# Optimization experiments

Hardware: AMD Instinct MI355X
Metric: run time of the kernel (lower is better)

The kernel has to match this reference:

```python
import jax, jax.numpy as jnp
import numpy as np

B, S, D, H = 2, 2048, 1024, 16
DK = D // H


def setup_inputs() -> dict:
    key = jax.random.key(0)
    ks = jax.random.split(key, 11)
    scale = jnp.float32(1.0 / np.sqrt(D))
    inp = {
        "query": jax.random.normal(ks[0], (B, S, D), jnp.float32),
        "key": jax.random.normal(ks[1], (B, S, D), jnp.float32),
        "value": jax.random.normal(ks[2], (B, S, D), jnp.float32),
        # causal mask: True = masked (masked_fill semantics), broadcast over batch/heads
        "mask": jnp.triu(jnp.ones((S, S), dtype=bool), k=1)[None, None, :, :],
        "Wq": jax.random.normal(ks[3], (D, D), jnp.float32) * scale,
        "bq": jnp.zeros((D,), jnp.float32),
        "Wk": jax.random.normal(ks[4], (D, D), jnp.float32) * scale,
        "bk": jnp.zeros((D,), jnp.float32),
        "Wv": jax.random.normal(ks[5], (D, D), jnp.float32) * scale,
        "bv": jnp.zeros((D,), jnp.float32),
        "Wo": jax.random.normal(ks[6], (D, D), jnp.float32) * scale,
        "bo": jnp.zeros((D,), jnp.float32),
    }
    return inp


def _split_heads(x):
    # (B, S, D) -> (B, H, S, DK)
    b, s, _ = x.shape
    return x.reshape(b, s, H, DK).transpose(0, 2, 1, 3)


def reference(query, key, value, mask, Wq, bq, Wk, bk, Wv, bv, Wo, bo):
    # nn.Linear: y = x @ W.T + b
    q = _split_heads(query @ Wq.T + bq)
    k = _split_heads(key @ Wk.T + bk)
    v = _split_heads(value @ Wv.T + bv)

    inv_sqrt_dk = jnp.float32(1.0 / np.sqrt(DK))
    scores = jnp.einsum("bhqd,bhkd->bhqk", q, k) * inv_sqrt_dk  # (B,H,S,S)
    scores = jnp.where(mask, jnp.float32(-jnp.inf), scores)
    weights = jax.nn.softmax(scores, axis=-1)
    weights = jnp.nan_to_num(weights, nan=0.0)  # fully-masked rows -> 0

    attn = jnp.einsum("bhqk,bhkd->bhqd", weights, v)  # (B,H,S,DK)
    merged = attn.transpose(0, 2, 1, 3).reshape(B, S, D)  # merge heads
    return merged @ Wo.T + bo
```

## Files before the change

kernel.cpp:

```cpp
#include <hip/hip_runtime.h>


typedef unsigned short u16;
typedef unsigned int u32;
typedef __attribute__((ext_vector_type(8))) __bf16 bf16x8;
typedef __attribute__((ext_vector_type(8))) unsigned short us8;
typedef __attribute__((ext_vector_type(4))) float f32x4;

#define S_LEN 2048
#define D_DIM 1024
#define NH 16
#define DKH 64
#define Mi 1048576ULL

__device__ __forceinline__ u16 f2bf(float f) {
  return __builtin_bit_cast(u16, (__bf16)f);
}
__device__ __forceinline__ bf16x8 ld_frag(const u16* p) {
  us8 v = *(const us8*)p;
  return __builtin_bit_cast(bf16x8, v);
}
__device__ __forceinline__ float fast_exp2(float x) {
  float r;
  asm("v_exp_f32 %0, %1" : "=v"(r) : "v"(x));
  return r;
}
__device__ __forceinline__ void gl2lds16(const u16* g, u16* l) {
  __builtin_amdgcn_global_load_lds(
      (__attribute__((address_space(1))) void*)(g),
      (__attribute__((address_space(3))) void*)(l), 16, 0, 0);
}

__global__ __launch_bounds__(256, 1) void cvt_all(
    const float* __restrict__ q, const float* __restrict__ k, const float* __restrict__ v,
    const float* __restrict__ wq, const float* __restrict__ wk,
    const float* __restrict__ wv, const float* __restrict__ wo,
    u16* __restrict__ dst, u32* __restrict__ cnt)
{
  if (blockIdx.x == 0 && threadIdx.x == 0) *cnt = 0;
  size_t e0 = ((size_t)blockIdx.x * 256 + threadIdx.x) * 8;
  const float* s;
  if      (e0 <  4*Mi) s = q  + e0;
  else if (e0 <  8*Mi) s = k  + (e0 - 4*Mi);
  else if (e0 < 12*Mi) s = v  + (e0 - 8*Mi);
  else if (e0 < 13*Mi) s = wq + (e0 - 12*Mi);
  else if (e0 < 14*Mi) s = wk + (e0 - 13*Mi);
  else if (e0 < 15*Mi) s = wv + (e0 - 14*Mi);
  else                 s = wo + (e0 - 15*Mi);
  float4 a = ((const float4*)s)[0];
  float4 b = ((const float4*)s)[1];
  us8 o;
  o[0]=f2bf(a.x); o[1]=f2bf(a.y); o[2]=f2bf(a.z); o[3]=f2bf(a.w);
  o[4]=f2bf(b.x); o[5]=f2bf(b.y); o[6]=f2bf(b.z); o[7]=f2bf(b.w);
  *(us8*)(dst + e0) = o;
}

__global__ __launch_bounds__(256, 1) void gemm_qkv_bb(
    const u16* __restrict__ Aq, const u16* __restrict__ Ak, const u16* __restrict__ Av,
    const u16* __restrict__ Wqb, const u16* __restrict__ Wkb, const u16* __restrict__ Wvb,
    const float* __restrict__ bq, const float* __restrict__ bk, const float* __restrict__ bv,
    u16* __restrict__ Oq, u16* __restrict__ Ok, u16* __restrict__ Ov, float qscale)
{
  const int z = blockIdx.z;
  const u16* A = (z == 0) ? Aq : (z == 1) ? Ak : Av;
  const u16* W = (z == 0) ? Wqb : (z == 1) ? Wkb : Wvb;
  const float* bias = (z == 0) ? bq : (z == 1) ? bk : bv;
  u16* out = (z == 0) ? Oq : (z == 1) ? Ok : Ov;
  const float scale = (z == 0) ? qscale : 1.0f;
  const int K = 1024;

  __shared__ u16 lA[128 * 32];
  __shared__ u16 lB[128 * 32];
  const int t = threadIdx.x;
  const int w = t >> 6, l = t & 63;
  const int mblk = blockIdx.y * 128, nblk = blockIdx.x * 128;
  const int wm = (w & 1) * 64, wn = (w >> 1) * 64;
  const int lr = l & 15, lq = l >> 4;
  const int srow = l >> 2, scol = (l & 3) * 8;

  f32x4 acc[4][4] = {};

  for (int k0 = 0; k0 < K; k0 += 32) {
    __syncthreads();
    #pragma unroll
    for (int r = 0; r < 2; ++r) {
      int grp = r * 4 + w;
      gl2lds16(A + (size_t)(mblk + grp * 16 + srow) * K + k0 + scol, &lA[grp * 512]);
      gl2lds16(W + (size_t)(nblk + grp * 16 + srow) * K + k0 + scol, &lB[grp * 512]);
    }
    __syncthreads();
    bf16x8 aF[4], bF[4];
    #pragma unroll
    for (int mt = 0; mt < 4; ++mt)
      aF[mt] = ld_frag(&lA[(wm + mt * 16 + lr) * 32 + lq * 8]);
    #pragma unroll
    for (int nt = 0; nt < 4; ++nt)
      bF[nt] = ld_frag(&lB[(wn + nt * 16 + lr) * 32 + lq * 8]);
    #pragma unroll
    for (int mt = 0; mt < 4; ++mt)
      #pragma unroll
      for (int nt = 0; nt < 4; ++nt)
        acc[mt][nt] = __builtin_amdgcn_mfma_f32_16x16x32_bf16(aF[mt], bF[nt], acc[mt][nt], 0, 0, 0);
  }

  #pragma unroll
  for (int mt = 0; mt < 4; ++mt)
    #pragma unroll
    for (int nt = 0; nt < 4; ++nt)
      #pragma unroll
      for (int r = 0; r < 4; ++r) {
        int rowg = mblk + wm + mt * 16 + lq * 4 + r;
        int colg = nblk + wn + nt * 16 + lr;
        float v = (acc[mt][nt][r] + bias[colg]) * scale;
        int b = rowg >> 11, s = rowg & 2047;
        int h = colg >> 6, dk = colg & 63;
        if (z != 2)
          out[(((size_t)(b * NH + h)) * S_LEN + s) * DKH + dk] = f2bf(v);
        else
          out[(((size_t)(b * NH + h)) * DKH + dk) * S_LEN + s] = f2bf(v);
      }
}

__global__ __launch_bounds__(256, 1) void gemm_out_bb(
    const u16* __restrict__ A, const u16* __restrict__ W,
    const float* __restrict__ bias, float* __restrict__ out)
{
  const int K = 1024;
  __shared__ u16 lA[128 * 64];
  __shared__ u16 lB[64 * 64];
  const int bid = blockIdx.x;
  const int o   = (bid & 7) * 64 + (bid >> 3);
  const int mblk = (o >> 4) * 128, nblk = (o & 15) * 64;
  const int t = threadIdx.x;
  const int w = t >> 6, l = t & 63;
  const int wm = (w & 1) * 64, wn = (w >> 1) * 32;
  const int lr = l & 15, lq = l >> 4;
  const int srow = l >> 3;
  const int sgr  = (l & 7) ^ srow;

  f32x4 acc[4][2] = {};

  for (int k0 = 0; k0 < K; k0 += 64) {
    __syncthreads();
    #pragma unroll
    for (int i = 0; i < 4; ++i) {
      int chunk = w * 4 + i;
      int row = chunk * 8 + srow;
      gl2lds16(A + (size_t)(mblk + row) * K + k0 + sgr * 8, &lA[chunk * 512]);
    }
    #pragma unroll
    for (int i = 0; i < 2; ++i) {
      int chunk = w * 2 + i;
      int row = chunk * 8 + srow;
      gl2lds16(W + (size_t)(nblk + row) * K + k0 + sgr * 8, &lB[chunk * 512]);
    }
    __syncthreads();
    #pragma unroll
    for (int kk = 0; kk < 2; ++kk) {
      bf16x8 aF[4], bF[2];
      #pragma unroll
      for (int mt = 0; mt < 4; ++mt)
        aF[mt] = ld_frag(&lA[(wm + mt * 16 + lr) * 64 + ((kk * 4 + lq) ^ (lr & 7)) * 8]);
      #pragma unroll
      for (int nt = 0; nt < 2; ++nt)
        bF[nt] = ld_frag(&lB[(wn + nt * 16 + lr) * 64 + ((kk * 4 + lq) ^ (lr & 7)) * 8]);
      #pragma unroll
      for (int mt = 0; mt < 4; ++mt)
        #pragma unroll
        for (int nt = 0; nt < 2; ++nt)
          acc[mt][nt] = __builtin_amdgcn_mfma_f32_16x16x32_bf16(aF[mt], bF[nt], acc[mt][nt], 0, 0, 0);
    }
  }

  #pragma unroll
  for (int mt = 0; mt < 4; ++mt)
    #pragma unroll
    for (int nt = 0; nt < 2; ++nt)
      #pragma unroll
      for (int r = 0; r < 4; ++r) {
        int rowg = mblk + wm + mt * 16 + lq * 4 + r;
        int colg = nblk + wn + nt * 16 + lr;
        out[(size_t)rowg * D_DIM + colg] = acc[mt][nt][r] + bias[colg];
      }
}

__global__ __launch_bounds__(256, 1) void attn_fused(
    const u16* __restrict__ Q, const u16* __restrict__ K,
    const u16* __restrict__ Vt, u16* __restrict__ O, u32* __restrict__ cnt)
{
  __shared__ u16 lK[3][64 * 64];
  __shared__ u16 lV[3][64 * 64];
  __shared__ int s_item;

  const int t = threadIdx.x;
  const int w = t >> 6, l = t & 63;
  const int lr = l & 15, lq = l >> 4;
  const int srow8 = l >> 3;
  const int schunk = l & 7;

  #define STAGE(T, bsel)                                                          \
    do {                                                                          \
      _Pragma("unroll")                                                           \
      for (int r2 = 0; r2 < 2; ++r2) {                                            \
        int grp = r2 * 4 + w;                                                     \
        int row = grp * 8 + srow8;                                                \
        int sw = (row & 3) | (((row >> 3) & 1) << 2);                             \
        int c = schunk ^ sw;                                                      \
        gl2lds16(Kp + (size_t)((T) * 64 + row) * DKH + c * 8, &lK[bsel][grp * 512]); \
        gl2lds16(Vp + (size_t)row * S_LEN + (T) * 64 + c * 8, &lV[bsel][grp * 512]); \
      }                                                                           \
    } while (0)

  while (true) {
    __syncthreads();
    if (t == 0) s_item = (int)atomicAdd(cnt, 1u);
    __syncthreads();
    const int item = s_item;
    if (item >= 1024) break;
    const int qt = 31 - (item >> 5);
    const int bh = item & 31;
    const int b = bh >> 4, h = bh & 15;

    const u16* Qp = Q + (size_t)bh * S_LEN * DKH;
    const u16* Kp = K + (size_t)bh * S_LEN * DKH;
    const u16* Vp = Vt + (size_t)bh * DKH * S_LEN;

    const int qrow = qt * 64 + w * 16 + lr;
    bf16x8 qf[2];
    qf[0] = ld_frag(Qp + (size_t)qrow * DKH + lq * 8);
    qf[1] = ld_frag(Qp + (size_t)qrow * DKH + 32 + lq * 8);

    f32x4 o4[4] = {};
    f32x4 li4 = {};

    STAGE(0, 0);
    if (qt >= 1) STAGE(1, 1);

    for (int kt = 0; kt < qt; ++kt) {
      const int cur = kt % 3;
      asm volatile("s_waitcnt vmcnt(4)\n\ts_barrier" ::: "memory");
      if (kt + 2 <= qt) STAGE(kt + 2, (kt + 2) % 3);

      f32x4 st[4] = {};
      #pragma unroll
      for (int ksd = 0; ksd < 2; ++ksd)
        #pragma unroll
        for (int nt = 0; nt < 4; ++nt) {
          int sig = 32 * (nt >> 1) + 8 * (lr >> 2) + 4 * (nt & 1) + (lr & 3);
          int slot = (ksd * 4 + lq) ^ (lr & 7);
          bf16x8 kb = ld_frag(&lK[cur][sig * 64 + slot * 8]);
          st[nt] = __builtin_amdgcn_mfma_f32_16x16x32_bf16(kb, qf[ksd], st[nt], 0, 0, 0);
        }

      float p[4][4];
      #pragma unroll
      for (int nt = 0; nt < 4; ++nt)
        #pragma unroll
        for (int r = 0; r < 4; ++r) {
          p[nt][r] = fast_exp2(st[nt][r]);
          li4[r] += p[nt][r];
        }

      #pragma unroll
      for (int ks = 0; ks < 2; ++ks) {
        us8 av;
        #pragma unroll
        for (int j = 0; j < 4; ++j) {
          av[j] = f2bf(p[2 * ks][j]);
          av[4 + j] = f2bf(p[2 * ks + 1][j]);
        }
        bf16x8 pa = __builtin_bit_cast(bf16x8, av);
        #pragma unroll
        for (int dblk = 0; dblk < 4; ++dblk) {
          int d = dblk * 16 + lr;
          int sw = (d & 3) | (((d >> 3) & 1) << 2);
          int slot = (4 * ks + lq) ^ sw;
          bf16x8 vb = ld_frag(&lV[cur][d * 64 + slot * 8]);
          o4[dblk] = __builtin_amdgcn_mfma_f32_16x16x32_bf16(pa, vb, o4[dblk], 0, 0, 0);
        }
      }
    }

    {
      const int cur = qt % 3;
      asm volatile("s_waitcnt vmcnt(0)\n\ts_barrier" ::: "memory");
      f32x4 st[4] = {};
      #pragma unroll
      for (int ksd = 0; ksd < 2; ++ksd)
        #pragma unroll
        for (int nt = 0; nt < 4; ++nt) {
          int sig = 32 * (nt >> 1) + 8 * (lr >> 2) + 4 * (nt & 1) + (lr & 3);
          int slot = (ksd * 4 + lq) ^ (lr & 7);
          bf16x8 kb = ld_frag(&lK[cur][sig * 64 + slot * 8]);
          st[nt] = __builtin_amdgcn_mfma_f32_16x16x32_bf16(kb, qf[ksd], st[nt], 0, 0, 0);
        }

      float p[4][4];
      const int qloc = w * 16 + lr;
      #pragma unroll
      for (int nt = 0; nt < 4; ++nt)
        #pragma unroll
        for (int r = 0; r < 4; ++r) {
          int kk = 32 * (nt >> 1) + 8 * lq + 4 * (nt & 1) + r;
          float e = fast_exp2(st[nt][r]);
          p[nt][r] = (kk > qloc) ? 0.0f : e;
          li4[r] += p[nt][r];
        }

      #pragma unroll
      for (int ks = 0; ks < 2; ++ks) {
        us8 av;
        #pragma unroll
        for (int j = 0; j < 4; ++j) {
          av[j] = f2bf(p[2 * ks][j]);
          av[4 + j] = f2bf(p[2 * ks + 1][j]);
        }
        bf16x8 pa = __builtin_bit_cast(bf16x8, av);
        #pragma unroll
        for (int dblk = 0; dblk < 4; ++dblk) {
          int d = dblk * 16 + lr;
          int sw = (d & 3) | (((d >> 3) & 1) << 2);
          int slot = (4 * ks + lq) ^ sw;
          bf16x8 vb = ld_frag(&lV[cur][d * 64 + slot * 8]);
          o4[dblk] = __builtin_amdgcn_mfma_f32_16x16x32_bf16(pa, vb, o4[dblk], 0, 0, 0);
        }
      }
    }

    float li = li4[0] + li4[1] + li4[2] + li4[3];
    li += __shfl_xor(li, 16);
    li += __shfl_xor(li, 32);
    float ri[4];
    #pragma unroll
    for (int r = 0; r < 4; ++r) ri[r] = 1.0f / __shfl(li, lq * 4 + r);

    const size_t obase = ((size_t)b * S_LEN + qt * 64 + w * 16) * D_DIM + h * DKH;
    #pragma unroll
    for (int dblk = 0; dblk < 4; ++dblk)
      #pragma unroll
      for (int r = 0; r < 4; ++r)
        O[obase + (size_t)(lq * 4 + r) * D_DIM + dblk * 16 + lr] = f2bf(o4[dblk][r] * ri[r]);
  }
  #undef STAGE
}

extern "C" void kernel_launch(void* const* d_in, const int* in_sizes, int n_in,
                              void* d_out, int out_size, void* d_ws, size_t ws_size,
                              hipStream_t stream) {
  const float* query = (const float*)d_in[0];
  const float* key   = (const float*)d_in[1];
  const float* value = (const float*)d_in[2];
  const float* Wq = (const float*)d_in[4];
  const float* bq = (const float*)d_in[5];
  const float* Wk = (const float*)d_in[6];
  const float* bk = (const float*)d_in[7];
  const float* Wv = (const float*)d_in[8];
  const float* bv = (const float*)d_in[9];
  const float* Wo = (const float*)d_in[10];
  const float* bo = (const float*)d_in[11];
  float* out = (float*)d_out;

  const float qscale = 0.125f * 1.44269504088896341f;
  dim3 blk(256);

  u16* base = (u16*)d_ws;
  u16* Qb = base;
  u16* Kb = base + 4 * Mi;
  u16* Vb = base + 8 * Mi;

  u16* cvt = base + 12 * Mi;
  u16* qbf = cvt;
  u16* kbf = cvt + 4 * Mi;
  u16* vbf = cvt + 8 * Mi;
  u16* wqb = cvt + 12 * Mi;
  u16* wkb = cvt + 13 * Mi;
  u16* wvb = cvt + 14 * Mi;
  u16* wob = cvt + 15 * Mi;
  u16* Ab  = qbf;

  u32* cnt = (u32*)d_out;

  cvt_all<<<dim3(8192), blk, 0, stream>>>(query, key, value, Wq, Wk, Wv, Wo, cvt, cnt);
  gemm_qkv_bb<<<dim3(8, 32, 3), blk, 0, stream>>>(qbf, kbf, vbf, wqb, wkb, wvb,
                                                  bq, bk, bv, Qb, Kb, Vb, qscale);
  attn_fused<<<dim3(768), blk, 0, stream>>>(Qb, Kb, Vb, Ab, cnt);
  gemm_out_bb<<<dim3(512), blk, 0, stream>>>(Ab, wob, bo, out);
}
```

Measured before the change: 230.6 us.

## Process paired query tiles per attention work item and remap QKV GEMM blocks

Each attention work item now handles two adjacent 64-row query tiles, so every staged K/V tile in LDS is reused by both query tiles. This halves the K/V global loads and barrier/sync overhead per query row. In exchange it doubles accumulator registers and coarsens the dynamic work items (512 instead of 1024), which can hurt load balance. The QKV GEMM grid is also flattened to 1D with a remapping that spreads consecutive block IDs across z and tiles, probably to spread the work across XCDs or improve cache locality.

```diff
diff --git a/kernel.cpp b/kernel.cpp
--- a/kernel.cpp
+++ b/kernel.cpp
@@ -61,7 +61,13 @@
     const float* __restrict__ bq, const float* __restrict__ bk, const float* __restrict__ bv,
     u16* __restrict__ Oq, u16* __restrict__ Ok, u16* __restrict__ Ov, float qscale)
 {
-  const int z = blockIdx.z;
+  const int bid = blockIdx.x;
+  const int o   = (bid & 7) * 96 + (bid >> 3);
+  const int z   = o >> 8;
+  const int rem = o & 255;
+  const int mblk = (rem >> 3) * 128;
+  const int nblk = (rem & 7) * 128;
+
   const u16* A = (z == 0) ? Aq : (z == 1) ? Ak : Av;
   const u16* W = (z == 0) ? Wqb : (z == 1) ? Wkb : Wvb;
   const float* bias = (z == 0) ? bq : (z == 1) ? bk : bv;
@@ -73,7 +79,6 @@
   __shared__ u16 lB[128 * 32];
   const int t = threadIdx.x;
   const int w = t >> 6, l = t & 63;
-  const int mblk = blockIdx.y * 128, nblk = blockIdx.x * 128;
   const int wm = (w & 1) * 64, wn = (w >> 1) * 64;
   const int lr = l & 15, lq = l >> 4;
   const int srow = l >> 2, scol = (l & 3) * 8;
@@ -211,37 +216,124 @@
       }                                                                           \
     } while (0)
 
+  #define QKT_PAIR(cur, stA, stB)                                                 \
+    do {                                                                          \
+      _Pragma("unroll")                                                           \
+      for (int ksd = 0; ksd < 2; ++ksd)                                           \
+        _Pragma("unroll")                                                         \
+        for (int nt = 0; nt < 4; ++nt) {                                          \
+          int sig = 32 * (nt >> 1) + 8 * (lr >> 2) + 4 * (nt & 1) + (lr & 3);     \
+          int slot = (ksd * 4 + lq) ^ (lr & 7);                                   \
+          bf16x8 kb = ld_frag(&lK[cur][sig * 64 + slot * 8]);                     \
+          stA[nt] = __builtin_amdgcn_mfma_f32_16x16x32_bf16(kb, qfA[ksd], stA[nt], 0, 0, 0); \
+          stB[nt] = __builtin_amdgcn_mfma_f32_16x16x32_bf16(kb, qfB[ksd], stB[nt], 0, 0, 0); \
+        }                                                                         \
+    } while (0)
+
+  #define PV_PAIR(cur, avA, avB)                                                  \
+    do {                                                                          \
+      _Pragma("unroll")                                                           \
+      for (int ks = 0; ks < 2; ++ks) {                                            \
+        bf16x8 paA = __builtin_bit_cast(bf16x8, avA[ks]);                         \
+        bf16x8 paB = __builtin_bit_cast(bf16x8, avB[ks]);                         \
+        _Pragma("unroll")                                                         \
+        for (int dblk = 0; dblk < 4; ++dblk) {                                    \
+          int d = dblk * 16 + lr;                                                 \
+          int sw = (d & 3) | (((d >> 3) & 1) << 2);                               \
+          int slot = (4 * ks + lq) ^ sw;                                          \
+          bf16x8 vb = ld_frag(&lV[cur][d * 64 + slot * 8]);                       \
+          o4A[dblk] = __builtin_amdgcn_mfma_f32_16x16x32_bf16(paA, vb, o4A[dblk], 0, 0, 0); \
+          o4B[dblk] = __builtin_amdgcn_mfma_f32_16x16x32_bf16(paB, vb, o4B[dblk], 0, 0, 0); \
+        }                                                                         \
+      }                                                                           \
+    } while (0)
+
   while (true) {
     __syncthreads();
     if (t == 0) s_item = (int)atomicAdd(cnt, 1u);
     __syncthreads();
     const int item = s_item;
-    if (item >= 1024) break;
-    const int qt = 31 - (item >> 5);
+    if (item >= 512) break;
+    const int j  = 15 - (item >> 5);
     const int bh = item & 31;
+    const int qta = 2 * j, qtb = 2 * j + 1;
     const int b = bh >> 4, h = bh & 15;
 
     const u16* Qp = Q + (size_t)bh * S_LEN * DKH;
     const u16* Kp = K + (size_t)bh * S_LEN * DKH;
     const u16* Vp = Vt + (size_t)bh * DKH * S_LEN;
 
-    const int qrow = qt * 64 + w * 16 + lr;
-    bf16x8 qf[2];
-    qf[0] = ld_frag(Qp + (size_t)qrow * DKH + lq * 8);
-    qf[1] = ld_frag(Qp + (size_t)qrow * DKH + 32 + lq * 8);
-
-    f32x4 o4[4] = {};
-    f32x4 li4 = {};
+    const int qrowA = qta * 64 + w * 16 + lr;
+    const int qrowB = qtb * 64 + w * 16 + lr;
+    bf16x8 qfA[2], qfB[2];
+    qfA[0] = ld_frag(Qp + (size_t)qrowA * DKH + lq * 8);
+    qfA[1] = ld_frag(Qp + (size_t)qrowA * DKH + 32 + lq * 8);
+    qfB[0] = ld_frag(Qp + (size_t)qrowB * DKH + lq * 8);
+    qfB[1] = ld_frag(Qp + (size_t)qrowB * DKH + 32 + lq * 8);
+
+    f32x4 o4A[4] = {}, o4B[4] = {};
+    f32x4 liA = {}, liB = {};
 
     STAGE(0, 0);
-    if (qt >= 1) STAGE(1, 1);
-
-    for (int kt = 0; kt < qt; ++kt) {
+    STAGE(1, 1);
+
+    for (int kt = 0; kt < qta; ++kt) {
       const int cur = kt % 3;
       asm volatile("s_waitcnt vmcnt(4)\n\ts_barrier" ::: "memory");
-      if (kt + 2 <= qt) STAGE(kt + 2, (kt + 2) % 3);
-
-      f32x4 st[4] = {};
+      if (kt + 2 <= qtb) STAGE(kt + 2, (kt + 2) % 3);
+
+      f32x4 stA[4] = {}, stB[4] = {};
+      QKT_PAIR(cur, stA, stB);
+
+      us8 avA[2], avB[2];
+      #pragma unroll
+      for (int ks = 0; ks < 2; ++ks)
+        #pragma unroll
+        for (int rr = 0; rr < 4; ++rr) {
+          float eA0 = fast_exp2(stA[2 * ks][rr]);
+          float eA1 = fast_exp2(stA[2 * ks + 1][rr]);
+          float eB0 = fast_exp2(stB[2 * ks][rr]);
+          float eB1 = fast_exp2(stB[2 * ks + 1][rr]);
+          liA[rr] += eA0 + eA1;
+          liB[rr] += eB0 + eB1;
+          avA[ks][rr] = f2bf(eA0); avA[ks][4 + rr] = f2bf(eA1);
+          avB[ks][rr] = f2bf(eB0); avB[ks][4 + rr] = f2bf(eB1);
+        }
+      PV_PAIR(cur, avA, avB);
+    }
+
+    {
+      const int cur = qta % 3;
+      asm volatile("s_waitcnt vmcnt(4)\n\ts_barrier" ::: "memory");
+
+      f32x4 stA[4] = {}, stB[4] = {};
+      QKT_PAIR(cur, stA, stB);
+
+      const int qloc = w * 16 + lr;
+      us8 avA[2], avB[2];
+      #pragma unroll
+      for (int ks = 0; ks < 2; ++ks)
+        #pragma unroll
+        for (int rr = 0; rr < 4; ++rr) {
+          int kk0 = 32 * ks + 8 * lq + rr;
+          int kk1 = 32 * ks + 8 * lq + 4 + rr;
+          float eA0 = (kk0 > qloc) ? 0.0f : fast_exp2(stA[2 * ks][rr]);
+          float eA1 = (kk1 > qloc) ? 0.0f : fast_exp2(stA[2 * ks + 1][rr]);
+          float eB0 = fast_exp2(stB[2 * ks][rr]);
+          float eB1 = fast_exp2(stB[2 * ks + 1][rr]);
+          liA[rr] += eA0 + eA1;
+          liB[rr] += eB0 + eB1;
+          avA[ks][rr] = f2bf(eA0); avA[ks][4 + rr] = f2bf(eA1);
+          avB[ks][rr] = f2bf(eB0); avB[ks][4 + rr] = f2bf(eB1);
+        }
+      PV_PAIR(cur, avA, avB);
+    }
+
+    {
+      const int cur = qtb % 3;
+      asm volatile("s_waitcnt vmcnt(0)\n\ts_barrier" ::: "memory");
+
+      f32x4 stB[4] = {};
       #pragma unroll
       for (int ksd = 0; ksd < 2; ++ksd)
         #pragma unroll
@@ -249,99 +341,62 @@
           int sig = 32 * (nt >> 1) + 8 * (lr >> 2) + 4 * (nt & 1) + (lr & 3);
           int slot = (ksd * 4 + lq) ^ (lr & 7);
           bf16x8 kb = ld_frag(&lK[cur][sig * 64 + slot * 8]);
-          st[nt] = __builtin_amdgcn_mfma_f32_16x16x32_bf16(kb, qf[ksd], st[nt], 0, 0, 0);
+          stB[nt] = __builtin_amdgcn_mfma_f32_16x16x32_bf16(kb, qfB[ksd], stB[nt], 0, 0, 0);
         }
 
-      float p[4][4];
-      #pragma unroll
-      for (int nt = 0; nt < 4; ++nt)
-        #pragma unroll
-        for (int r = 0; r < 4; ++r) {
-          p[nt][r] = fast_exp2(st[nt][r]);
-          li4[r] += p[nt][r];
+      const int qloc = w * 16 + lr;
+      us8 avB[2];
+      #pragma unroll
+      for (int ks = 0; ks < 2; ++ks)
+        #pragma unroll
+        for (int rr = 0; rr < 4; ++rr) {
+          int kk0 = 32 * ks + 8 * lq + rr;
+          int kk1 = 32 * ks + 8 * lq + 4 + rr;
+          float eB0 = (kk0 > qloc) ? 0.0f : fast_exp2(stB[2 * ks][rr]);
+          float eB1 = (kk1 > qloc) ? 0.0f : fast_exp2(stB[2 * ks + 1][rr]);
+          liB[rr] += eB0 + eB1;
+          avB[ks][rr] = f2bf(eB0); avB[ks][4 + rr] = f2bf(eB1);
         }
-
       #pragma unroll
       for (int ks = 0; ks < 2; ++ks) {
-        us8 av;
-        #pragma unroll
-        for (int j = 0; j < 4; ++j) {
-          av[j] = f2bf(p[2 * ks][j]);
-          av[4 + j] = f2bf(p[2 * ks + 1][j]);
-        }
-        bf16x8 pa = __builtin_bit_cast(bf16x8, av);
+        bf16x8 paB = __builtin_bit_cast(bf16x8, avB[ks]);
         #pragma unroll
         for (int dblk = 0; dblk < 4; ++dblk) {
           int d = dblk * 16 + lr;
           int sw = (d & 3) | (((d >> 3) & 1) << 2);
           int slot = (4 * ks + lq) ^ sw;
           bf16x8 vb = ld_frag(&lV[cur][d * 64 + slot * 8]);
-          o4[dblk] = __builtin_amdgcn_mfma_f32_16x16x32_bf16(pa, vb, o4[dblk], 0, 0, 0);
+          o4B[dblk] = __builtin_amdgcn_mfma_f32_16x16x32_bf16(paB, vb, o4B[dblk], 0, 0, 0);
         }
       }
     }
 
-    {
-      const int cur = qt % 3;
-      asm volatile("s_waitcnt vmcnt(0)\n\ts_barrier" ::: "memory");
-      f32x4 st[4] = {};
-      #pragma unroll
-      for (int ksd = 0; ksd < 2; ++ksd)
-        #pragma unroll
-        for (int nt = 0; nt < 4; ++nt) {
-          int sig = 32 * (nt >> 1) + 8 * (lr >> 2) + 4 * (nt & 1) + (lr & 3);
-          int slot = (ksd * 4 + lq) ^ (lr & 7);
-          bf16x8 kb = ld_frag(&lK[cur][sig * 64 + slot * 8]);
-          st[nt] = __builtin_amdgcn_mfma_f32_16x16x32_bf16(kb, qf[ksd], st[nt], 0, 0, 0);
-        }
-
-      float p[4][4];
-      const int qloc = w * 16 + lr;
-      #pragma unroll
-      for (int nt = 0; nt < 4; ++nt)
-        #pragma unroll
-        for (int r = 0; r < 4; ++r) {
-          int kk = 32 * (nt >> 1) + 8 * lq + 4 * (nt & 1) + r;
-          float e = fast_exp2(st[nt][r]);
-          p[nt][r] = (kk > qloc) ? 0.0f : e;
-          li4[r] += p[nt][r];
-        }
-
-      #pragma unroll
-      for (int ks = 0; ks < 2; ++ks) {
-        us8 av;
-        #pragma unroll
-        for (int j = 0; j < 4; ++j) {
-          av[j] = f2bf(p[2 * ks][j]);
-          av[4 + j] = f2bf(p[2 * ks + 1][j]);
-        }
-        bf16x8 pa = __builtin_bit_cast(bf16x8, av);
-        #pragma unroll
-        for (int dblk = 0; dblk < 4; ++dblk) {
-          int d = dblk * 16 + lr;
-          int sw = (d & 3) | (((d >> 3) & 1) << 2);
-          int slot = (4 * ks + lq) ^ sw;
-          bf16x8 vb = ld_frag(&lV[cur][d * 64 + slot * 8]);
-          o4[dblk] = __builtin_amdgcn_mfma_f32_16x16x32_bf16(pa, vb, o4[dblk], 0, 0, 0);
-        }
+    float lA_ = liA[0] + liA[1] + liA[2] + liA[3];
+    lA_ += __shfl_xor(lA_, 16);
+    lA_ += __shfl_xor(lA_, 32);
+    float lB_ = liB[0] + liB[1] + liB[2] + liB[3];
+    lB_ += __shfl_xor(lB_, 16);
+    lB_ += __shfl_xor(lB_, 32);
+    float riA[4], riB[4];
+    #pragma unroll
+    for (int r = 0; r < 4; ++r) {
+      riA[r] = 1.0f / __shfl(lA_, lq * 4 + r);
+      riB[r] = 1.0f / __shfl(lB_, lq * 4 + r);
+    }
+
+    const size_t obaseA = ((size_t)b * S_LEN + qta * 64 + w * 16) * D_DIM + h * DKH;
+    const size_t obaseB = ((size_t)b * S_LEN + qtb * 64 + w * 16) * D_DIM + h * DKH;
+    #pragma unroll
+    for (int dblk = 0; dblk < 4; ++dblk)
+      #pragma unroll
+      for (int r = 0; r < 4; ++r) {
+        O[obaseA + (size_t)(lq * 4 + r) * D_DIM + dblk * 16 + lr] = f2bf(o4A[dblk][r] * riA[r]);
+        O[obaseB + (size_t)(lq * 4 + r) * D_DIM + dblk * 16 + lr] = f2bf(o4B[dblk][r] * riB[r]);
       }
-    }
-
-    float li = li4[0] + li4[1] + li4[2] + li4[3];
-    li += __shfl_xor(li, 16);
-    li += __shfl_xor(li, 32);
-    float ri[4];
-    #pragma unroll
-    for (int r = 0; r < 4; ++r) ri[r] = 1.0f / __shfl(li, lq * 4 + r);
-
-    const size_t obase = ((size_t)b * S_LEN + qt * 64 + w * 16) * D_DIM + h * DKH;
-    #pragma unroll
-    for (int dblk = 0; dblk < 4; ++dblk)
-      #pragma unroll
-      for (int r = 0; r < 4; ++r)
-        O[obase + (size_t)(lq * 4 + r) * D_DIM + dblk * 16 + lr] = f2bf(o4[dblk][r] * ri[r]);
   }
   #undef STAGE
+  #undef QKT_PAIR
+  #undef PV_PAIR
 }
 
 extern "C" void kernel_launch(void* const* d_in, const int* in_sizes, int n_in,
@@ -381,8 +436,8 @@
   u32* cnt = (u32*)d_out;
 
   cvt_all<<<dim3(8192), blk, 0, stream>>>(query, key, value, Wq, Wk, Wv, Wo, cvt, cnt);
-  gemm_qkv_bb<<<dim3(8, 32, 3), blk, 0, stream>>>(qbf, kbf, vbf, wqb, wkb, wvb,
-                                                  bq, bk, bv, Qb, Kb, Vb, qscale);
+  gemm_qkv_bb<<<dim3(768), blk, 0, stream>>>(qbf, kbf, vbf, wqb, wkb, wvb,
+                                             bq, bk, bv, Qb, Kb, Vb, qscale);
   attn_fused<<<dim3(768), blk, 0, stream>>>(Qb, Kb, Vb, Ab, cnt);
   gemm_out_bb<<<dim3(512), blk, 0, stream>>>(Ab, wob, bo, out);
 }
```

New measurement: 248.4 us. +7.7%, slower.

## Prefetch next attention work item's Q and first K/V tiles during diagonal tile

Applied to the files above, without the earlier changes.

The persistent attention loop now grabs the next work-item index with an atomic one item ahead. During the current item's diagonal (masked) tile it loads the next item's Q fragments and stages its first two K/V tiles into the free LDS buffers. A rotating buffer base replaces the fixed kt%3 indexing, so the triple buffer carries across items and the per-item prologue stall and double barrier go away. The cost is more bookkeeping, more live registers for the next Q fragments, and an unconditional second-tile prefetch even when qt is 0.

```diff
diff --git a/kernel.cpp b/kernel.cpp
--- a/kernel.cpp
+++ b/kernel.cpp
@@ -190,7 +190,7 @@
 {
   __shared__ u16 lK[3][64 * 64];
   __shared__ u16 lV[3][64 * 64];
-  __shared__ int s_item;
+  __shared__ int s_item[2];
 
   const int t = threadIdx.x;
   const int w = t >> 6, l = t & 63;
@@ -198,48 +198,56 @@
   const int srow8 = l >> 3;
   const int schunk = l & 7;
 
-  #define STAGE(T, bsel)                                                          \
-    do {                                                                          \
-      _Pragma("unroll")                                                           \
-      for (int r2 = 0; r2 < 2; ++r2) {                                            \
-        int grp = r2 * 4 + w;                                                     \
-        int row = grp * 8 + srow8;                                                \
-        int sw = (row & 3) | (((row >> 3) & 1) << 2);                             \
-        int c = schunk ^ sw;                                                      \
-        gl2lds16(Kp + (size_t)((T) * 64 + row) * DKH + c * 8, &lK[bsel][grp * 512]); \
-        gl2lds16(Vp + (size_t)row * S_LEN + (T) * 64 + c * 8, &lV[bsel][grp * 512]); \
-      }                                                                           \
+  #define STAGE(KP, VP, T, bsel)                                                   \
+    do {                                                                           \
+      _Pragma("unroll")                                                            \
+      for (int r2 = 0; r2 < 2; ++r2) {                                             \
+        int grp = r2 * 4 + w;                                                      \
+        int row = grp * 8 + srow8;                                                 \
+        int sw = (row & 3) | (((row >> 3) & 1) << 2);                              \
+        int c = schunk ^ sw;                                                       \
+        gl2lds16((KP) + (size_t)((T) * 64 + row) * DKH + c * 8, &lK[bsel][grp * 512]); \
+        gl2lds16((VP) + (size_t)row * S_LEN + (T) * 64 + c * 8, &lV[bsel][grp * 512]); \
+      }                                                                            \
     } while (0)
 
+  if (t == 0) s_item[0] = (int)atomicAdd(cnt, 1u);
+  __syncthreads();
+  int item = s_item[0];
+  if (item >= 1024) return;
+  int phase = 0;
+  int qt = 31 - (item >> 5);
+  int bh = item & 31;
+  int b = bh >> 4, h = bh & 15;
+
+  const u16* Kp = K + (size_t)bh * S_LEN * DKH;
+  const u16* Vp = Vt + (size_t)bh * DKH * S_LEN;
+  {
+    const u16* Qp = Q + (size_t)bh * S_LEN * DKH;
+    int qrow = qt * 64 + w * 16 + lr;
+    (void)qrow;
+  }
+  bf16x8 qf0, qf1;
+  {
+    const u16* Qp = Q + (size_t)bh * S_LEN * DKH;
+    int qrow = qt * 64 + w * 16 + lr;
+    qf0 = ld_frag(Qp + (size_t)qrow * DKH + lq * 8);
+    qf1 = ld_frag(Qp + (size_t)qrow * DKH + 32 + lq * 8);
+  }
+  u32 nxt_raw = 0;
+  if (t == 0) nxt_raw = atomicAdd(cnt, 1u);
+  STAGE(Kp, Vp, 0, 0);
+  STAGE(Kp, Vp, 1, 1);
+  int base = 0;
+
   while (true) {
-    __syncthreads();
-    if (t == 0) s_item = (int)atomicAdd(cnt, 1u);
-    __syncthreads();
-    const int item = s_item;
-    if (item >= 1024) break;
-    const int qt = 31 - (item >> 5);
-    const int bh = item & 31;
-    const int b = bh >> 4, h = bh & 15;
-
-    const u16* Qp = Q + (size_t)bh * S_LEN * DKH;
-    const u16* Kp = K + (size_t)bh * S_LEN * DKH;
-    const u16* Vp = Vt + (size_t)bh * DKH * S_LEN;
-
-    const int qrow = qt * 64 + w * 16 + lr;
-    bf16x8 qf[2];
-    qf[0] = ld_frag(Qp + (size_t)qrow * DKH + lq * 8);
-    qf[1] = ld_frag(Qp + (size_t)qrow * DKH + 32 + lq * 8);
-
     f32x4 o4[4] = {};
     f32x4 li4 = {};
 
-    STAGE(0, 0);
-    if (qt >= 1) STAGE(1, 1);
-
     for (int kt = 0; kt < qt; ++kt) {
-      const int cur = kt % 3;
+      const int cur = (base + kt) % 3;
       asm volatile("s_waitcnt vmcnt(4)\n\ts_barrier" ::: "memory");
-      if (kt + 2 <= qt) STAGE(kt + 2, (kt + 2) % 3);
+      if (kt + 2 <= qt) STAGE(Kp, Vp, kt + 2, (base + kt + 2) % 3);
 
       f32x4 st[4] = {};
       #pragma unroll
@@ -249,7 +257,7 @@
           int sig = 32 * (nt >> 1) + 8 * (lr >> 2) + 4 * (nt & 1) + (lr & 3);
           int slot = (ksd * 4 + lq) ^ (lr & 7);
           bf16x8 kb = ld_frag(&lK[cur][sig * 64 + slot * 8]);
-          st[nt] = __builtin_amdgcn_mfma_f32_16x16x32_bf16(kb, qf[ksd], st[nt], 0, 0, 0);
+          st[nt] = __builtin_amdgcn_mfma_f32_16x16x32_bf16(kb, (ksd == 0) ? qf0 : qf1, st[nt], 0, 0, 0);
         }
 
       float p[4][4];
@@ -281,9 +289,30 @@
       }
     }
 
+    const int dsel = (base + qt) % 3;
+    if (t == 0) s_item[phase ^ 1] = (int)nxt_raw;
+    asm volatile("s_waitcnt vmcnt(0)\n\ts_barrier" ::: "memory");
+    const int nitem = s_item[phase ^ 1];
+    const bool have_next = (nitem < 1024);
+
+    int nqt = 0, nbh = 0, nbase = 0;
+    const u16 *Kn = nullptr, *Vn = nullptr;
+    bf16x8 qfN0 = {}, qfN1 = {};
+    if (have_next) {
+      nqt = 31 - (nitem >> 5);
+      nbh = nitem & 31;
+      const u16* Qn = Q + (size_t)nbh * S_LEN * DKH;
+      Kn = K + (size_t)nbh * S_LEN * DKH;
+      Vn = Vt + (size_t)nbh * DKH * S_LEN;
+      int nqrow = nqt * 64 + w * 16 + lr;
+      qfN0 = ld_frag(Qn + (size_t)nqrow * DKH + lq * 8);
+      qfN1 = ld_frag(Qn + (size_t)nqrow * DKH + 32 + lq * 8);
+      nbase = (base + qt + 1) % 3;
+      STAGE(Kn, Vn, 0, nbase);
+      STAGE(Kn, Vn, 1, (nbase + 1) % 3);
+    }
+
     {
-      const int cur = qt % 3;
-      asm volatile("s_waitcnt vmcnt(0)\n\ts_barrier" ::: "memory");
       f32x4 st[4] = {};
       #pragma unroll
       for (int ksd = 0; ksd < 2; ++ksd)
@@ -291,8 +320,8 @@
         for (int nt = 0; nt < 4; ++nt) {
           int sig = 32 * (nt >> 1) + 8 * (lr >> 2) + 4 * (nt & 1) + (lr & 3);
           int slot = (ksd * 4 + lq) ^ (lr & 7);
-          bf16x8 kb = ld_frag(&lK[cur][sig * 64 + slot * 8]);
-          st[nt] = __builtin_amdgcn_mfma_f32_16x16x32_bf16(kb, qf[ksd], st[nt], 0, 0, 0);
+          bf16x8 kb = ld_frag(&lK[dsel][sig * 64 + slot * 8]);
+          st[nt] = __builtin_amdgcn_mfma_f32_16x16x32_bf16(kb, (ksd == 0) ? qf0 : qf1, st[nt], 0, 0, 0);
         }
 
       float p[4][4];
@@ -321,7 +350,7 @@
           int d = dblk * 16 + lr;
           int sw = (d & 3) | (((d >> 3) & 1) << 2);
           int slot = (4 * ks + lq) ^ sw;
-          bf16x8 vb = ld_frag(&lV[cur][d * 64 + slot * 8]);
+          bf16x8 vb = ld_frag(&lV[dsel][d * 64 + slot * 8]);
           o4[dblk] = __builtin_amdgcn_mfma_f32_16x16x32_bf16(pa, vb, o4[dblk], 0, 0, 0);
         }
       }
@@ -340,6 +369,12 @@
       #pragma unroll
       for (int r = 0; r < 4; ++r)
         O[obase + (size_t)(lq * 4 + r) * D_DIM + dblk * 16 + lr] = f2bf(o4[dblk][r] * ri[r]);
+
+    if (!have_next) break;
+    qt = nqt; bh = nbh; b = bh >> 4; h = bh & 15;
+    Kp = Kn; Vp = Vn; qf0 = qfN0; qf1 = qfN1;
+    base = nbase; phase ^= 1;
+    if (t == 0) nxt_raw = atomicAdd(cnt, 1u);
   }
   #undef STAGE
 }
```

Result: slower. 246.2 us (+6.7%).
